# Performance work log

Measured on AMD Instinct MI355X. Metric: run time of the kernel, lower is better.

The kernel has to match this reference:

```python
import jax, jax.numpy as jnp
import numpy as np

B, D, H4, L, T, VOCAB, DMID = 256, 512, 2048, 3, 201, 128, 1024
START_IDX = 0


def setup_inputs() -> dict:
    key = jax.random.key(0)
    ks = jax.random.split(key, 8)
    s = lambda k, shape, scale=0.02: jax.random.normal(k, shape, jnp.float32) * scale
    return {
        "feat": jax.random.normal(ks[0], (B, D), jnp.float32),
        "Wvis": s(ks[1], (D, D)),
        "bvis": jnp.zeros((D,), jnp.float32),
        "embed": s(ks[2], (VOCAB, D)),
        "Wih": s(ks[3], (L, H4, D)),
        "Whh": s(ks[4], (L, H4, D)),
        "bih": jnp.zeros((L, H4), jnp.float32),
        "bhh": jnp.zeros((L, H4), jnp.float32),
        "W1": s(ks[5], (DMID, D)),
        "b1": jnp.zeros((DMID,), jnp.float32),
        "W2": s(ks[6], (VOCAB, DMID)),
        "b2": jnp.zeros((VOCAB,), jnp.float32),
    }


def reference(feat, Wvis, bvis, embed, Wih, Whh, bih, bhh, W1, b1, W2, b2):
    # visual_proj applied once in forward(), then again per-layer in _init_hidden
    feat_p = feat @ Wvis.T + bvis                    # [B,D]
    h0_layer = feat_p @ Wvis.T + bvis                # same for every layer
    h0 = jnp.tile(h0_layer[None], (L, 1, 1))         # [L,B,D]
    c0 = jnp.zeros_like(h0)
    inp0 = jnp.broadcast_to(embed[START_IDX], (B, D))  # embed(<sos>)

    def step(carry, _):
        inp, h, c = carry
        x = inp
        hs, cs = [], []
        for l in range(L):  # small fixed layer count
            g = x @ Wih[l].T + bih[l] + h[l] @ Whh[l].T + bhh[l]  # [B,4D]
            i, f, gg, o = jnp.split(g, 4, axis=-1)  # torch gate order i,f,g,o
            c_l = jax.nn.sigmoid(f) * c[l] + jax.nn.sigmoid(i) * jnp.tanh(gg)
            h_l = jax.nn.sigmoid(o) * jnp.tanh(c_l)
            hs.append(h_l)
            cs.append(c_l)
            x = h_l
        out = x  # top-layer output; dropout is identity in eval
        # inp = out.detach() in the original loop
        return (jax.lax.stop_gradient(out), jnp.stack(hs), jnp.stack(cs)), out

    _, outs = jax.lax.scan(step, (inp0, h0, c0), None, length=T)  # [T,B,D]
    res = outs.transpose(1, 0, 2)                                 # [B,T,D]
    mid = jax.nn.gelu(res @ W1.T + b1, approximate=False)         # torch GELU is erf-exact
    logits = mid @ W2.T + b2                                      # [B,T,V]
    return logits.transpose(0, 2, 1)                              # [B,V,T]
```

## Files before the change

### kernel.cpp

```cpp
#include <hip/hip_runtime.h>

#define NB   256
#define ND   512
#define NH4  2048
#define NL   3
#define NT   201
#define NV   128
#define NMID 1024

typedef _Float16 half8 __attribute__((ext_vector_type(8)));
typedef float f32x4 __attribute__((ext_vector_type(4)));

__device__ __forceinline__ float sigf(float x) { return 1.0f / (1.0f + __expf(-x)); }
__device__ __forceinline__ float tanh_(float x) {
  float e = __expf(-2.0f * fabsf(x));
  float t = (1.0f - e) / (1.0f + e);
  return x < 0.0f ? -t : t;
}

__device__ __forceinline__ half8 l2_load(const _Float16* p) {
  half8 v;
  asm volatile("global_load_dwordx4 %0, %1, off sc0" : "=v"(v) : "v"(p));
  return v;
}

__device__ __forceinline__ unsigned l2_rmw_add(unsigned* p, unsigned val) {
  unsigned v;
  asm volatile("global_atomic_add %0, %1, %2, off sc0\n\ts_waitcnt vmcnt(0)"
               : "=v"(v) : "v"(p), "v"(val) : "memory");
  return v;
}

__device__ __forceinline__ void xbar(unsigned* cnt, bool pref) {
  if (pref && threadIdx.x >= 256)
    asm volatile("s_waitcnt vmcnt(8)" ::: "memory");
  else
    asm volatile("s_waitcnt vmcnt(0)" ::: "memory");
  __syncthreads();
  if (threadIdx.x == 0) {
    unsigned old = l2_rmw_add(cnt, 1u);
    unsigned target = (old & ~31u) + 32u;
    int guard = 1 << 16;
    while (l2_rmw_add(cnt, 0u) < target && --guard)
      __builtin_amdgcn_s_sleep(1);
  }
  __syncthreads();
  asm volatile("buffer_inv" ::: "memory");
  __builtin_amdgcn_sched_barrier(0);
}


__global__ void prep_w(const float* __restrict__ Wih, const float* __restrict__ Whh,
                       const float* __restrict__ bih, const float* __restrict__ bhh,
                       _Float16* __restrict__ Wp, float* __restrict__ bp) {
  size_t idx = (size_t)blockIdx.x * 256 + threadIdx.x;
  {
    int k = (int)(idx & 1023);
    int R = (int)((idx >> 10) & 2047);
    int l = (int)(idx >> 21);
    int dt = R >> 6, g = (R >> 4) & 3, di = R & 15;
    int col = g * 512 + dt * 16 + di;
    float v = (k < 512) ? Wih[((size_t)l * NH4 + col) * ND + k]
                        : Whh[((size_t)l * NH4 + col) * ND + (k - 512)];
    Wp[idx] = (_Float16)v;
  }
  if (idx < (size_t)NL * NH4) {
    int R = (int)(idx & 2047);
    int l = (int)(idx >> 11);
    int dt = R >> 6, g = (R >> 4) & 3, di = R & 15;
    int col = g * 512 + dt * 16 + di;
    bp[idx] = bih[l * NH4 + col] + bhh[l * NH4 + col];
  }
}

__global__ void prep_misc(const float* __restrict__ Wvis, const float* __restrict__ feat,
                          const float* __restrict__ embed, const float* __restrict__ W1,
                          const float* __restrict__ W2,
                          _Float16* __restrict__ Wvis16, _Float16* __restrict__ feat16,
                          _Float16* __restrict__ x0, _Float16* __restrict__ W1h,
                          _Float16* __restrict__ W2h, unsigned* __restrict__ cnt) {
  int idx = blockIdx.x * 256 + threadIdx.x;
  if (idx < 512 * 512)  Wvis16[idx] = (_Float16)Wvis[idx];
  if (idx < 256 * 512)  feat16[idx] = (_Float16)feat[idx];
  if (idx < 256 * 512)  x0[idx]     = (_Float16)embed[idx & 511];
  if (idx < 1024 * 512) W1h[idx]    = (_Float16)W1[idx];
  if (idx < 128 * 1024) W2h[idx]    = (_Float16)W2[idx];
  if (idx < 1024) cnt[idx] = 0;
}

__global__ __launch_bounds__(512, 2) void lstm_persist(
    const _Float16* __restrict__ Wp,
    const float* __restrict__ bp,
    const _Float16* __restrict__ Wvis,
    const float* __restrict__ bvis,
    const _Float16* __restrict__ feat16,
    const _Float16* __restrict__ x0,
    _Float16* __restrict__ featp,
    _Float16* __restrict__ hbuf,
    _Float16* __restrict__ res,
    unsigned* __restrict__ cntbase) {
  __shared__ _Float16 wlds[64][1024];
  __shared__ float expart[4][4][16][32];

  const int tid = threadIdx.x;
  const int lane = tid & 63, w = tid >> 6;
  const int lr = lane & 15, lg = (lane >> 4) & 3;

  unsigned xcd;
  asm volatile("s_getreg_b32 %0, hwreg(HW_REG_XCC_ID)" : "=s"(xcd));
  xcd &= 7u;

  unsigned* rank_slot = (unsigned*)&expart[0][0][0][0];
  if (tid == 0)
    *rank_slot = __hip_atomic_fetch_add(cntbase + 256 + xcd * 32, 1u,
                                        __ATOMIC_RELAXED, __HIP_MEMORY_SCOPE_AGENT);
  __syncthreads();
  const int rank = (int)(*rank_slot & 31u);
  __syncthreads();

  const int dt = rank;
  const int m0 = (int)xcd * 32;
  const int d0 = rank * 16;
  unsigned* cnt = cntbase + xcd * 32;

  #pragma unroll 4
  for (int i = 0; i < 16; ++i) {
    int G = tid + 512 * i;
    int r = G >> 7, g = G & 127;
    *(half8*)&wlds[r][(g ^ (r & 7)) * 8] =
        *(const half8*)(Wp + ((size_t)(dt * 64 + r)) * 1024 + g * 8);
  }
  half8 wreg[2][4][4];
  #pragma unroll
  for (int ly = 0; ly < 2; ++ly)
    #pragma unroll
    for (int n = 0; n < 4; ++n)
      #pragma unroll
      for (int kk = 0; kk < 4; ++kk)
        wreg[ly][n][kk] = *(const half8*)(Wp +
          ((size_t)((ly + 1) * NH4 + dt * 64 + n * 16 + lr)) * 1024 + w * 128 + kk * 32 + lg * 8);

  const int di = tid & 15, cb = (tid >> 4) & 31;
  float breg[3][4];
  #pragma unroll
  for (int l = 0; l < 3; ++l)
    #pragma unroll
    for (int g = 0; g < 4; ++g)
      breg[l][g] = bp[l * NH4 + dt * 64 + g * 16 + di];

  {
    float* xb = &expart[0][0][0][0];
    const int wm2 = w & 1, wk = w >> 1;
    #pragma unroll 1
    for (int pg = 0; pg < 2; ++pg) {
      const _Float16* A = pg ? featp : feat16;
      half8 avp[4];
      #pragma unroll
      for (int kc = 0; kc < 4; ++kc)
        avp[kc] = l2_load(A + (size_t)(m0 + wm2 * 16 + lr) * ND + wk * 128 + kc * 32 + lg * 8);
      asm volatile("s_waitcnt vmcnt(0)" ::: "memory");
      __builtin_amdgcn_sched_barrier(0);
      f32x4 pacc = {0.f, 0.f, 0.f, 0.f};
      #pragma unroll
      for (int kc = 0; kc < 4; ++kc) {
        half8 bb = *(const half8*)(Wvis + (size_t)(d0 + lr) * ND + wk * 128 + kc * 32 + lg * 8);
        pacc = __builtin_amdgcn_mfma_f32_16x16x32_f16(avp[kc], bb, pacc, 0, 0, 0);
      }
      #pragma unroll
      for (int j = 0; j < 4; ++j)
        xb[wk * 512 + (wm2 * 16 + lg * 4 + j) * 16 + lr] = pacc[j];
      __syncthreads();
      {
        int m = tid >> 4, d = tid & 15;
        float v = xb[m * 16 + d] + xb[512 + m * 16 + d] + xb[1024 + m * 16 + d]
                + xb[1536 + m * 16 + d] + bvis[d0 + d];
        _Float16 hv = (_Float16)v;
        size_t off = (size_t)(m0 + m) * ND + d0 + d;
        if (pg == 0) featp[off] = hv;
        else {
          hbuf[(size_t)(0 * 2 + 1) * (NB * ND) + off] = hv;
          hbuf[(size_t)(1 * 2 + 1) * (NB * ND) + off] = hv;
          hbuf[(size_t)(2 * 2 + 1) * (NB * ND) + off] = hv;
        }
      }
      xbar(cnt, false);
    }
  }

  float cst[3] = {0.f, 0.f, 0.f};
  const size_t aoff0 = (size_t)(m0 + lr) * ND + (size_t)(w & 3) * 128 + lg * 8;
  const size_t aoff1 = aoff0 + (size_t)16 * ND;
  half8 av0[4], av1[4];

  #pragma unroll 1
  for (int t = 0; t < NT; ++t) {
    #pragma unroll
    for (int l = 0; l < 3; ++l) {
      const _Float16* xsrc = (l == 0)
        ? ((t == 0) ? x0 : hbuf + (size_t)(2 * 2 + ((t + 1) & 1)) * (NB * ND))
        : hbuf + (size_t)((l - 1) * 2 + (t & 1)) * (NB * ND);
      const _Float16* hsrc = hbuf + (size_t)(l * 2 + ((t + 1) & 1)) * (NB * ND);
      _Float16* hdst       = hbuf + (size_t)(l * 2 + (t & 1)) * (NB * ND);

      if (w < 4) {
        #pragma unroll
        for (int kk = 0; kk < 4; ++kk) {
          av0[kk] = l2_load(xsrc + aoff0 + kk * 32);
          av1[kk] = l2_load(xsrc + aoff1 + kk * 32);
        }
      } else if (t == 0 && l == 0) {
        #pragma unroll
        for (int kk = 0; kk < 4; ++kk) {
          av0[kk] = l2_load(hsrc + aoff0 + kk * 32);
          av1[kk] = l2_load(hsrc + aoff1 + kk * 32);
        }
      }
      asm volatile("s_waitcnt vmcnt(0)" ::: "memory");
      __builtin_amdgcn_sched_barrier(0);

      f32x4 acc[2][4];
      #pragma unroll
      for (int m = 0; m < 2; ++m)
        #pragma unroll
        for (int n = 0; n < 4; ++n)
          acc[m][n] = (f32x4){0.f, 0.f, 0.f, 0.f};

      if (l == 0) {
        #pragma unroll
        for (int kk = 0; kk < 4; ++kk) {
          int kg = w * 16 + kk * 4 + lg;
          #pragma unroll
          for (int n = 0; n < 4; ++n) {
            half8 bf = *(const half8*)&wlds[n * 16 + lr][(kg ^ (lr & 7)) * 8];
            acc[0][n] = __builtin_amdgcn_mfma_f32_16x16x32_f16(av0[kk], bf, acc[0][n], 0, 0, 0);
            acc[1][n] = __builtin_amdgcn_mfma_f32_16x16x32_f16(av1[kk], bf, acc[1][n], 0, 0, 0);
          }
        }
      } else {
        #pragma unroll
        for (int kk = 0; kk < 4; ++kk)
          #pragma unroll
          for (int n = 0; n < 4; ++n) {
            half8 bf = wreg[l - 1][n][kk];
            acc[0][n] = __builtin_amdgcn_mfma_f32_16x16x32_f16(av0[kk], bf, acc[0][n], 0, 0, 0);
            acc[1][n] = __builtin_amdgcn_mfma_f32_16x16x32_f16(av1[kk], bf, acc[1][n], 0, 0, 0);
          }
      }

      if (w >= 4) {
        #pragma unroll
        for (int m = 0; m < 2; ++m)
          #pragma unroll
          for (int n = 0; n < 4; ++n) {
            int pos = (m * 16 + lg * 4 + lr * 4) & 31;
            *(f32x4*)&expart[w - 4][n][lr][pos] = acc[m][n];
          }
      }
      __syncthreads();
      if (w < 4) {
        #pragma unroll
        for (int m = 0; m < 2; ++m)
          #pragma unroll
          for (int n = 0; n < 4; ++n) {
            int pos = (m * 16 + lg * 4 + lr * 4) & 31;
            f32x4* pp = (f32x4*)&expart[w][n][lr][pos];
            f32x4 tv = *pp;
            tv += acc[m][n];
            *pp = tv;
          }
      }
      __syncthreads();

      {
        int bq = (cb + di * 4) & 31;
        float s0 = expart[0][0][di][bq] + expart[1][0][di][bq] + expart[2][0][di][bq] + expart[3][0][di][bq];
        float s1 = expart[0][1][di][bq] + expart[1][1][di][bq] + expart[2][1][di][bq] + expart[3][1][di][bq];
        float s2 = expart[0][2][di][bq] + expart[1][2][di][bq] + expart[2][2][di][bq] + expart[3][2][di][bq];
        float s3 = expart[0][3][di][bq] + expart[1][3][di][bq] + expart[2][3][di][bq] + expart[3][3][di][bq];
        float gi = s0 + breg[l][0];
        float gf = s1 + breg[l][1];
        float gg = s2 + breg[l][2];
        float go = s3 + breg[l][3];
        float c = cst[l];
        c = sigf(gf) * c + sigf(gi) * tanh_(gg);
        cst[l] = c;
        _Float16 hv = (_Float16)(sigf(go) * tanh_(c));
        size_t off = (size_t)(m0 + cb) * ND + d0 + di;
        hdst[off] = hv;
        if (l == 2) res[(size_t)t * (NB * ND) + off] = hv;
      }

      if (!(t == NT - 1 && l == 2)) {
        if (w >= 4) {
          const int nt2 = (l == 2) ? t + 1 : t;
          const int nl  = (l == 2) ? 0 : l + 1;
          const _Float16* nh = hbuf + (size_t)(nl * 2 + ((nt2 + 1) & 1)) * (NB * ND);
          #pragma unroll
          for (int kk = 0; kk < 4; ++kk) {
            av0[kk] = l2_load(nh + aoff0 + kk * 32);
            av1[kk] = l2_load(nh + aoff1 + kk * 32);
          }
        }
        xbar(cnt, true);
      }
    }
  }
}

__global__ __launch_bounds__(256, 2) void head_kernel(
    const _Float16* __restrict__ res,
    const _Float16* __restrict__ W1h,
    const float* __restrict__ b1,
    const _Float16* __restrict__ W2h,
    const float* __restrict__ b2,
    float* __restrict__ out) {
  const int tile = blockIdx.x;
  const int tid = threadIdx.x;
  const int lane = tid & 63, w = tid >> 6;
  const int lr = lane & 15, lg = lane >> 4;
  const int r0 = tile * 64;

  __shared__ _Float16 mid[64][128];

  f32x4 acc2[8];
  #pragma unroll
  for (int n = 0; n < 8; ++n) acc2[n] = (f32x4){0.f, 0.f, 0.f, 0.f};

  const size_t arow = (size_t)(r0 + w * 16 + lr) * ND;

  #pragma unroll 1
  for (int nc = 0; nc < 8; ++nc) {
    f32x4 acc1[8];
    #pragma unroll
    for (int n = 0; n < 8; ++n) acc1[n] = (f32x4){0.f, 0.f, 0.f, 0.f};
    #pragma unroll 2
    for (int kc = 0; kc < 16; ++kc) {
      half8 a = *(const half8*)(res + arow + kc * 32 + lg * 8);
      #pragma unroll
      for (int n = 0; n < 8; ++n) {
        half8 bb = *(const half8*)(W1h + (size_t)(nc * 128 + n * 16 + lr) * ND + kc * 32 + lg * 8);
        acc1[n] = __builtin_amdgcn_mfma_f32_16x16x32_f16(a, bb, acc1[n], 0, 0, 0);
      }
    }
    __syncthreads();
    #pragma unroll
    for (int n = 0; n < 8; ++n) {
      #pragma unroll
      for (int j = 0; j < 4; ++j) {
        int m = w * 16 + lg * 4 + j;
        int col = n * 16 + lr;
        float v = acc1[n][j] + b1[nc * 128 + col];
        v = 0.5f * v * (1.0f + erff(v * 0.7071067811865475f));
        int sw = (((col >> 3) ^ (m & 15)) << 3) + (col & 7);
        mid[m][sw] = (_Float16)v;
      }
    }
    __syncthreads();
    #pragma unroll
    for (int kc2 = 0; kc2 < 4; ++kc2) {
      int row = w * 16 + lr;
      int blk = (kc2 * 4 + lg) ^ (row & 15);
      half8 a2 = *(const half8*)(&mid[row][blk * 8]);
      #pragma unroll
      for (int n = 0; n < 8; ++n) {
        half8 bb = *(const half8*)(W2h + (size_t)(n * 16 + lr) * NMID + nc * 128 + kc2 * 32 + lg * 8);
        acc2[n] = __builtin_amdgcn_mfma_f32_16x16x32_f16(a2, bb, acc2[n], 0, 0, 0);
      }
    }
  }
  #pragma unroll
  for (int n = 0; n < 8; ++n) {
    #pragma unroll
    for (int j = 0; j < 4; ++j) {
      int r = r0 + w * 16 + lg * 4 + j;
      int b = r & 255, t = r >> 8;
      int v = n * 16 + lr;
      out[((size_t)b * NV + v) * NT + t] = acc2[n][j] + b2[v];
    }
  }
}

extern "C" void kernel_launch(void* const* d_in, const int* in_sizes, int n_in,
                              void* d_out, int out_size, void* d_ws, size_t ws_size,
                              hipStream_t stream) {
  const float* feat  = (const float*)d_in[0];
  const float* Wvis  = (const float*)d_in[1];
  const float* bvis  = (const float*)d_in[2];
  const float* embed = (const float*)d_in[3];
  const float* Wih   = (const float*)d_in[4];
  const float* Whh   = (const float*)d_in[5];
  const float* bih   = (const float*)d_in[6];
  const float* bhh   = (const float*)d_in[7];
  const float* W1    = (const float*)d_in[8];
  const float* b1    = (const float*)d_in[9];
  const float* W2    = (const float*)d_in[10];
  const float* b2    = (const float*)d_in[11];
  float* out = (float*)d_out;

  char* p = (char*)d_ws;
  _Float16* Wp     = (_Float16*)p; p += (size_t)NL * NH4 * 1024 * 2;
  _Float16* Wvis16 = (_Float16*)p; p += (size_t)512 * 512 * 2;
  _Float16* feat16 = (_Float16*)p; p += (size_t)256 * 512 * 2;
  _Float16* x0     = (_Float16*)p; p += (size_t)256 * 512 * 2;
  _Float16* featp  = (_Float16*)p; p += (size_t)256 * 512 * 2;
  _Float16* hbuf   = (_Float16*)p; p += (size_t)NL * 2 * NB * ND * 2;
  _Float16* resb   = (_Float16*)p; p += (size_t)NT * NB * ND * 2;
  _Float16* W1h    = (_Float16*)p; p += (size_t)NMID * ND * 2;
  _Float16* W2h    = (_Float16*)p; p += (size_t)NV * NMID * 2;
  float*    bp     = (float*)p;    p += (size_t)NL * NH4 * 4;
  unsigned* cnt    = (unsigned*)p; p += 4096;

  prep_w<<<24576, 256, 0, stream>>>(Wih, Whh, bih, bhh, Wp, bp);
  prep_misc<<<2048, 256, 0, stream>>>(Wvis, feat, embed, W1, W2,
                                      Wvis16, feat16, x0, W1h, W2h, cnt);
  lstm_persist<<<256, 512, 0, stream>>>(Wp, bp, Wvis16, bvis, feat16, x0,
                                        featp, hbuf, resb, cnt);
  head_kernel<<<804, 256, 0, stream>>>(resb, W1h, b1, W2h, b2, out);
  (void)in_sizes; (void)n_in; (void)out_size; (void)ws_size;
}
```

Measured before the change: 2.919 ms.

## Split grid barrier into arrive/wait and overlap recurrent h-GEMM during wait

Splits the software grid barrier into an arrive phase and a wait phase. Warps 4-7 run the recurrent-state (h) GEMM for the next layer and prefetch its operands in the gap between the two, so that work overlaps the barrier latency. Warps 0-3 preload half of the layer-0 LDS weight fragments into registers during that gap. The x-side GEMM is split into two halves with a partial vmcnt wait so compute starts before all loads land. The cost is higher register pressure, more complex inter-warp synchronisation, and a longer spin-sleep interval.

```diff
diff --git a/kernel.cpp b/kernel.cpp
--- a/kernel.cpp
+++ b/kernel.cpp
@@ -31,18 +31,21 @@
   return v;
 }
 
-__device__ __forceinline__ void xbar(unsigned* cnt, bool pref) {
-  if (pref && threadIdx.x >= 256)
-    asm volatile("s_waitcnt vmcnt(8)" ::: "memory");
-  else
-    asm volatile("s_waitcnt vmcnt(0)" ::: "memory");
+__device__ __forceinline__ unsigned bar_arrive(unsigned* cnt) {
+  asm volatile("s_waitcnt vmcnt(0)" ::: "memory");
   __syncthreads();
+  unsigned target = 0;
   if (threadIdx.x == 0) {
     unsigned old = l2_rmw_add(cnt, 1u);
-    unsigned target = (old & ~31u) + 32u;
+    target = (old & ~31u) + 32u;
+  }
+  return target;
+}
+__device__ __forceinline__ void bar_wait(unsigned* cnt, unsigned target) {
+  if (threadIdx.x == 0) {
     int guard = 1 << 16;
     while (l2_rmw_add(cnt, 0u) < target && --guard)
-      __builtin_amdgcn_s_sleep(1);
+      __builtin_amdgcn_s_sleep(2);
   }
   __syncthreads();
   asm volatile("buffer_inv" ::: "memory");
@@ -147,6 +150,8 @@
     #pragma unroll
     for (int g = 0; g < 4; ++g)
       breg[l][g] = bp[l * NH4 + dt * 64 + g * 16 + di];
+
+  half8 bl0[2][4];
 
   {
     float* xb = &expart[0][0][0][0];
@@ -183,7 +188,17 @@
           hbuf[(size_t)(2 * 2 + 1) * (NB * ND) + off] = hv;
         }
       }
-      xbar(cnt, false);
+      unsigned bt = bar_arrive(cnt);
+      if (pg == 1 && w < 4) {
+        #pragma unroll
+        for (int kk = 0; kk < 2; ++kk)
+          #pragma unroll
+          for (int n = 0; n < 4; ++n) {
+            int kg = w * 16 + kk * 4 + lg;
+            bl0[kk][n] = *(const half8*)&wlds[n * 16 + lr][(kg ^ (lr & 7)) * 8];
+          }
+      }
+      bar_wait(cnt, bt);
     }
   }
 
@@ -196,6 +211,8 @@
   for (int t = 0; t < NT; ++t) {
     #pragma unroll
     for (int l = 0; l < 3; ++l) {
+      const bool first = (t == 0 && l == 0);
+      const bool last  = (t == NT - 1 && l == 2);
       const _Float16* xsrc = (l == 0)
         ? ((t == 0) ? x0 : hbuf + (size_t)(2 * 2 + ((t + 1) & 1)) * (NB * ND))
         : hbuf + (size_t)((l - 1) * 2 + (t & 1)) * (NB * ND);
@@ -204,60 +221,48 @@
 
       if (w < 4) {
         #pragma unroll
-        for (int kk = 0; kk < 4; ++kk) {
-          av0[kk] = l2_load(xsrc + aoff0 + kk * 32);
-          av1[kk] = l2_load(xsrc + aoff1 + kk * 32);
+        for (int kk = 0; kk < 4; ++kk) av0[kk] = l2_load(xsrc + aoff0 + kk * 32);
+        #pragma unroll
+        for (int kk = 0; kk < 4; ++kk) av1[kk] = l2_load(xsrc + aoff1 + kk * 32);
+
+        half8 bl23[2][4];
+        if (l == 0) {
+          #pragma unroll
+          for (int kk = 0; kk < 2; ++kk)
+            #pragma unroll
+            for (int n = 0; n < 4; ++n) {
+              int kg = w * 16 + (kk + 2) * 4 + lg;
+              bl23[kk][n] = *(const half8*)&wlds[n * 16 + lr][(kg ^ (lr & 7)) * 8];
+            }
         }
-      } else if (t == 0 && l == 0) {
-        #pragma unroll
-        for (int kk = 0; kk < 4; ++kk) {
-          av0[kk] = l2_load(hsrc + aoff0 + kk * 32);
-          av1[kk] = l2_load(hsrc + aoff1 + kk * 32);
-        }
-      }
-      asm volatile("s_waitcnt vmcnt(0)" ::: "memory");
-      __builtin_amdgcn_sched_barrier(0);
-
-      f32x4 acc[2][4];
-      #pragma unroll
-      for (int m = 0; m < 2; ++m)
-        #pragma unroll
-        for (int n = 0; n < 4; ++n)
-          acc[m][n] = (f32x4){0.f, 0.f, 0.f, 0.f};
-
-      if (l == 0) {
-        #pragma unroll
-        for (int kk = 0; kk < 4; ++kk) {
-          int kg = w * 16 + kk * 4 + lg;
+        f32x4 acc[2][4];
+        #pragma unroll
+        for (int m = 0; m < 2; ++m)
+          #pragma unroll
+          for (int n = 0; n < 4; ++n) acc[m][n] = (f32x4){0.f, 0.f, 0.f, 0.f};
+
+        asm volatile("s_waitcnt vmcnt(4)" ::: "memory");
+        __builtin_amdgcn_sched_barrier(0);
+        #pragma unroll
+        for (int kk = 0; kk < 4; ++kk)
           #pragma unroll
           for (int n = 0; n < 4; ++n) {
-            half8 bf = *(const half8*)&wlds[n * 16 + lr][(kg ^ (lr & 7)) * 8];
+            half8 bf = (l == 0) ? (kk < 2 ? bl0[kk][n] : bl23[kk - 2][n])
+                                : wreg[l - 1][n][kk];
             acc[0][n] = __builtin_amdgcn_mfma_f32_16x16x32_f16(av0[kk], bf, acc[0][n], 0, 0, 0);
+          }
+        asm volatile("s_waitcnt vmcnt(0)" ::: "memory");
+        __builtin_amdgcn_sched_barrier(0);
+        #pragma unroll
+        for (int kk = 0; kk < 4; ++kk)
+          #pragma unroll
+          for (int n = 0; n < 4; ++n) {
+            half8 bf = (l == 0) ? (kk < 2 ? bl0[kk][n] : bl23[kk - 2][n])
+                                : wreg[l - 1][n][kk];
             acc[1][n] = __builtin_amdgcn_mfma_f32_16x16x32_f16(av1[kk], bf, acc[1][n], 0, 0, 0);
           }
-        }
-      } else {
-        #pragma unroll
-        for (int kk = 0; kk < 4; ++kk)
-          #pragma unroll
-          for (int n = 0; n < 4; ++n) {
-            half8 bf = wreg[l - 1][n][kk];
-            acc[0][n] = __builtin_amdgcn_mfma_f32_16x16x32_f16(av0[kk], bf, acc[0][n], 0, 0, 0);
-            acc[1][n] = __builtin_amdgcn_mfma_f32_16x16x32_f16(av1[kk], bf, acc[1][n], 0, 0, 0);
-          }
-      }
-
-      if (w >= 4) {
-        #pragma unroll
-        for (int m = 0; m < 2; ++m)
-          #pragma unroll
-          for (int n = 0; n < 4; ++n) {
-            int pos = (m * 16 + lg * 4 + lr * 4) & 31;
-            *(f32x4*)&expart[w - 4][n][lr][pos] = acc[m][n];
-          }
-      }
-      __syncthreads();
-      if (w < 4) {
+
+        if (first) __syncthreads();
         #pragma unroll
         for (int m = 0; m < 2; ++m)
           #pragma unroll
@@ -268,6 +273,41 @@
             tv += acc[m][n];
             *pp = tv;
           }
+      } else if (first) {
+        #pragma unroll
+        for (int kk = 0; kk < 4; ++kk) av0[kk] = l2_load(hsrc + aoff0 + kk * 32);
+        #pragma unroll
+        for (int kk = 0; kk < 4; ++kk) av1[kk] = l2_load(hsrc + aoff1 + kk * 32);
+        asm volatile("s_waitcnt vmcnt(0)" ::: "memory");
+        __builtin_amdgcn_sched_barrier(0);
+        f32x4 acc[2][4];
+        #pragma unroll
+        for (int m = 0; m < 2; ++m)
+          #pragma unroll
+          for (int n = 0; n < 4; ++n) acc[m][n] = (f32x4){0.f, 0.f, 0.f, 0.f};
+        #pragma unroll
+        for (int kk = 0; kk < 4; ++kk)
+          #pragma unroll
+          for (int n = 0; n < 4; ++n) {
+            int kg = w * 16 + kk * 4 + lg;
+            half8 bf = *(const half8*)&wlds[n * 16 + lr][(kg ^ (lr & 7)) * 8];
+            acc[0][n] = __builtin_amdgcn_mfma_f32_16x16x32_f16(av0[kk], bf, acc[0][n], 0, 0, 0);
+            acc[1][n] = __builtin_amdgcn_mfma_f32_16x16x32_f16(av1[kk], bf, acc[1][n], 0, 0, 0);
+          }
+        #pragma unroll
+        for (int m = 0; m < 2; ++m)
+          #pragma unroll
+          for (int n = 0; n < 4; ++n) {
+            int pos = (m * 16 + lg * 4 + lr * 4) & 31;
+            *(f32x4*)&expart[w - 4][n][lr][pos] = acc[m][n];
+          }
+        const _Float16* nh = hbuf + (size_t)(1 * 2 + 1) * (NB * ND);
+        #pragma unroll
+        for (int kk = 0; kk < 4; ++kk) {
+          av0[kk] = l2_load(nh + aoff0 + kk * 32);
+          av1[kk] = l2_load(nh + aoff1 + kk * 32);
+        }
+        __syncthreads();
       }
       __syncthreads();
 
@@ -290,18 +330,60 @@
         if (l == 2) res[(size_t)t * (NB * ND) + off] = hv;
       }
 
-      if (!(t == NT - 1 && l == 2)) {
+      if (!last) {
+        unsigned bt = bar_arrive(cnt);
+
         if (w >= 4) {
-          const int nt2 = (l == 2) ? t + 1 : t;
-          const int nl  = (l == 2) ? 0 : l + 1;
-          const _Float16* nh = hbuf + (size_t)(nl * 2 + ((nt2 + 1) & 1)) * (NB * ND);
-          #pragma unroll
-          for (int kk = 0; kk < 4; ++kk) {
-            av0[kk] = l2_load(nh + aoff0 + kk * 32);
-            av1[kk] = l2_load(nh + aoff1 + kk * 32);
-          }
+          asm volatile("s_waitcnt vmcnt(0)" ::: "memory");
+          __builtin_amdgcn_sched_barrier(0);
+          f32x4 hacc[2][4];
+          #pragma unroll
+          for (int m = 0; m < 2; ++m)
+            #pragma unroll
+            for (int n = 0; n < 4; ++n) hacc[m][n] = (f32x4){0.f, 0.f, 0.f, 0.f};
+          #pragma unroll
+          for (int kk = 0; kk < 4; ++kk)
+            #pragma unroll
+            for (int n = 0; n < 4; ++n) {
+              half8 bf;
+              if (l == 2) {
+                int kg = w * 16 + kk * 4 + lg;
+                bf = *(const half8*)&wlds[n * 16 + lr][(kg ^ (lr & 7)) * 8];
+              } else {
+                bf = wreg[l][n][kk];
+              }
+              hacc[0][n] = __builtin_amdgcn_mfma_f32_16x16x32_f16(av0[kk], bf, hacc[0][n], 0, 0, 0);
+              hacc[1][n] = __builtin_amdgcn_mfma_f32_16x16x32_f16(av1[kk], bf, hacc[1][n], 0, 0, 0);
+            }
+          #pragma unroll
+          for (int m = 0; m < 2; ++m)
+            #pragma unroll
+            for (int n = 0; n < 4; ++n) {
+              int pos = (m * 16 + lg * 4 + lr * 4) & 31;
+              *(f32x4*)&expart[w - 4][n][lr][pos] = hacc[m][n];
+            }
+          if (!(t == NT - 1 && l == 1)) {
+            const _Float16* nh =
+              (l == 0) ? hbuf + (size_t)(2 * 2 + ((t + 1) & 1)) * (NB * ND) :
+              (l == 1) ? hbuf + (size_t)(0 * 2 + (t & 1)) * (NB * ND)
+                       : hbuf + (size_t)(1 * 2 + (t & 1)) * (NB * ND);
+            #pragma unroll
+            for (int kk = 0; kk < 4; ++kk) {
+              av0[kk] = l2_load(nh + aoff0 + kk * 32);
+              av1[kk] = l2_load(nh + aoff1 + kk * 32);
+            }
+          }
+        } else if (l == 2) {
+          #pragma unroll
+          for (int kk = 0; kk < 2; ++kk)
+            #pragma unroll
+            for (int n = 0; n < 4; ++n) {
+              int kg = w * 16 + kk * 4 + lg;
+              bl0[kk][n] = *(const half8*)&wlds[n * 16 + lr][(kg ^ (lr & 7)) * 8];
+            }
         }
-        xbar(cnt, true);
+
+        bar_wait(cnt, bt);
       }
     }
   }
```

Measured after the change: 3.559 ms. 1.22x slower.
